# Kernel tuning notes

Hardware: AMD Instinct MI355X
Metric: run time of the kernel (lower is better)

Reference implementation:

```python
import jax, jax.numpy as jnp
import numpy as np

B, T, C = 8, 2048, 768
N_LAYER, LAYER_ID = 12, 0


def setup_inputs() -> dict:
    key = jax.random.key(0)
    ks = jax.random.split(key, 5)
    s = 1.0 / np.sqrt(C)
    x = jax.random.normal(ks[0], (B, T, C), jnp.float32)
    Wk = jax.random.normal(ks[1], (C, C), jnp.float32) * s
    Wv = jax.random.normal(ks[2], (C, C), jnp.float32) * s
    Wr = jax.random.normal(ks[3], (C, C), jnp.float32) * s
    Wo = jax.random.normal(ks[4], (C, C), jnp.float32) * s
    # 'fancy' init for decay / first (layer_id=0 -> ratio_0_to_1 = 0)
    h = np.arange(C, dtype=np.float64)
    decay = (-5.0 + 8.0 * (h / (C - 1)) ** 0.7).astype(np.float32)
    zigzag = (((np.arange(C) + 1) % 3) - 1).astype(np.float64) * 0.5
    first = (np.log(0.3) + zigzag).astype(np.float32)
    return dict(x=x, Wk=Wk, Wv=Wv, Wr=Wr, Wo=Wo,
                decay=jnp.asarray(decay), first=jnp.asarray(first))


def _bi_wkv(w, u, k, v):
    """Bidirectional WKV (Vision-RWKV style), numerically stabilized scans.

    y_t = (sum_{i<t} e^{-(t-1-i)w + k_i} v_i + sum_{i>t} e^{-(i-1-t)w + k_i} v_i
           + e^{u + k_t} v_t) / (same with v_i -> 1).
    k, v: [B,T,C]; w, u: [C].
    """
    kT = jnp.swapaxes(k, 0, 1)  # [T,B,C]
    vT = jnp.swapaxes(v, 0, 1)
    Bb, Cc = kT.shape[1], kT.shape[2]
    NEG = jnp.float32(-1e38)

    def step(carry, inp):
        a, b, p = carry  # a = sum e^{x_i-p} v_i, b = sum e^{x_i-p}, p = running max
        kt, vt = inp
        out = (a, b, p)  # state covers strictly-earlier positions
        p_new = jnp.maximum(p - w, kt)
        e1 = jnp.exp(p - w - p_new)
        e2 = jnp.exp(kt - p_new)
        return (e1 * a + e2 * vt, e1 * b + e2, p_new), out

    init = (jnp.zeros((Bb, Cc), jnp.float32),
            jnp.zeros((Bb, Cc), jnp.float32),
            jnp.full((Bb, Cc), NEG, jnp.float32))
    _, (aL, bL, pL) = jax.lax.scan(step, init, (kT, vT))
    _, (aR, bR, pR) = jax.lax.scan(step, init, (kT[::-1], vT[::-1]))
    aR, bR, pR = aR[::-1], bR[::-1], pR[::-1]

    ps = u + kT  # self term exponent
    q = jnp.maximum(jnp.maximum(pL, pR), ps)
    eL = jnp.exp(pL - q)
    eR = jnp.exp(pR - q)
    eS = jnp.exp(ps - q)
    y = (eL * aL + eR * aR + eS * vT) / (eL * bL + eR * bR + eS)
    return jnp.swapaxes(y, 0, 1)  # [B,T,C]


def reference(x, Wk, Wv, Wr, Wo, decay, first):
    Tlen = x.shape[1]
    # shift_pixel=0 -> xk = xv = xr = x
    k = jnp.einsum('btc,oc->bto', x, Wk)
    v = jnp.einsum('btc,oc->bto', x, Wv)
    sr = jax.nn.sigmoid(jnp.einsum('btc,oc->bto', x, Wr))
    y = _bi_wkv(decay / Tlen, first / Tlen, k, v)
    return jnp.einsum('btj,cj->btc', sr * y, Wo)
```

## Files before the change

### kernel.cpp

```cpp
#include <hip/hip_runtime.h>

#define BSZ 8
#define TLEN 2048
#define CDIM 768
#define LCH 16
#define NCH (TLEN / LCH)

typedef __attribute__((ext_vector_type(4))) float f32x4;
typedef __attribute__((ext_vector_type(8))) _Float16 f16x8;
typedef __attribute__((ext_vector_type(4))) _Float16 f16x4;
typedef __attribute__((ext_vector_type(4))) float float4v;

#define GLD16(g, l)                                                          \
    __builtin_amdgcn_global_load_lds(                                        \
        (const __attribute__((address_space(1))) unsigned int*)(g),          \
        (__attribute__((address_space(3))) unsigned int*)(l), 16, 0, 0)

__global__ __launch_bounds__(256) void split_f16(const float* __restrict__ src,
                                                 _Float16* __restrict__ dst, int n4) {
    int i = blockIdx.x * 256 + threadIdx.x;
    if (i >= n4) return;
    float4v f = ((const float4v*)src)[i];
    f16x4 h;
    #pragma unroll
    for (int j = 0; j < 4; ++j) h[j] = (_Float16)f[j];
    ((f16x4*)dst)[i] = h;
}

__global__ __launch_bounds__(512, 2) void gemm_8ph(
    const _Float16* __restrict__ A, const _Float16* __restrict__ W,
    _Float16* __restrict__ o0, _Float16* __restrict__ o1, _Float16* __restrict__ o2,
    float* __restrict__ of32, int mpx, int NTL) {
    constexpr int K = CDIM;
    constexpr int NT = K / 64;
    __shared__ __align__(16) char smem[131072];

    const int tid  = threadIdx.x;
    const int lane = tid & 63;
    const int wid  = tid >> 6;
    const int bid  = blockIdx.x;
    const int xcd  = bid & 7;
    const int lj   = bid >> 3;
    const int mt   = lj / NTL;
    const int nt   = lj - mt * NTL;
    const int m0   = (xcd * mpx + mt) * 256;
    const int n0   = nt * 256;

    const int r0 = tid >> 3;
    const int c0 = (tid & 7) ^ (r0 & 7);
    const int s1 = tid + 512;
    const int r1 = s1 >> 3;
    const int c1 = (s1 & 7) ^ (r1 & 7);
    const char* gA = (const char*)A;
    const char* gW = (const char*)W;

    auto STAGE_HALF = [&](int bufb, int q, int t) {
        const bool isA = (q < 2);
        const char* g = isA ? gA : gW;
        const int rowb = (isA ? m0 : n0) + (q & 1) * 128;
        char* l = &smem[bufb + q * 16384];
        GLD16(g + (size_t)((rowb + r0) * (K * 2) + c0 * 16 + t * 128), l + tid * 16);
        GLD16(g + (size_t)((rowb + r1) * (K * 2) + c1 * 16 + t * 128), l + s1 * 16);
    };

    const int wr = wid >> 2;
    const int wc = wid & 3;
    const int rl = lane & 15;
    const int kc0 = (((lane >> 4)    ) ^ (rl & 7)) << 4;
    const int kc1 = (((lane >> 4) + 4) ^ (rl & 7)) << 4;

    f32x4 acc[8][4];
    #pragma unroll
    for (int i = 0; i < 8; ++i)
        #pragma unroll
        for (int j = 0; j < 4; ++j)
            acc[i][j] = (f32x4){0.f, 0.f, 0.f, 0.f};

    #pragma unroll
    for (int q = 0; q < 4; ++q) STAGE_HALF(0, q, 0);
    asm volatile("s_waitcnt vmcnt(0)" ::: "memory");
    __builtin_amdgcn_s_barrier();

    for (int t = 0; t < NT; ++t) {
        const int db  = (t & 1) << 16;
        const int nb2 = db ^ 65536;
        const char* sb = &smem[db];
        f16x8 breg[4][2];

        #pragma unroll
        for (int q = 0; q < 4; ++q) {
            f16x8 areg[2][2];
            #pragma unroll
            for (int mi = 0; mi < 2; ++mi) {
                const int ro = (wr * 128 + (2 * q + mi) * 16 + rl) * 128;
                areg[mi][0] = *(const f16x8*)(sb + ro + kc0);
                areg[mi][1] = *(const f16x8*)(sb + ro + kc1);
            }
            if (q == 0) {
                #pragma unroll
                for (int nf = 0; nf < 4; ++nf) {
                    const int ro = 32768 + (wc * 64 + nf * 16 + rl) * 128;
                    breg[nf][0] = *(const f16x8*)(sb + ro + kc0);
                    breg[nf][1] = *(const f16x8*)(sb + ro + kc1);
                }
            }
            if (t + 1 < NT) STAGE_HALF(nb2, q, t + 1);

            __builtin_amdgcn_s_barrier();
            asm volatile("s_waitcnt lgkmcnt(0)" ::: "memory");
            __builtin_amdgcn_sched_barrier(0);
            __builtin_amdgcn_s_setprio(1);
            #pragma unroll
            for (int mi = 0; mi < 2; ++mi)
                #pragma unroll
                for (int nf = 0; nf < 4; ++nf) {
                    acc[2 * q + mi][nf] = __builtin_amdgcn_mfma_f32_16x16x32_f16(
                        areg[mi][0], breg[nf][0], acc[2 * q + mi][nf], 0, 0, 0);
                    acc[2 * q + mi][nf] = __builtin_amdgcn_mfma_f32_16x16x32_f16(
                        areg[mi][1], breg[nf][1], acc[2 * q + mi][nf], 0, 0, 0);
                }
            __builtin_amdgcn_s_setprio(0);
            if (q == 3) asm volatile("s_waitcnt vmcnt(0)" ::: "memory");
            __builtin_amdgcn_s_barrier();
        }
    }

    const int erow0 = m0 + wr * 128 + ((lane >> 4) << 2);
    if (of32) {
        const int col0 = n0 + wc * 64 + rl;
        #pragma unroll
        for (int mf = 0; mf < 8; ++mf)
            #pragma unroll
            for (int nf = 0; nf < 4; ++nf)
                #pragma unroll
                for (int r = 0; r < 4; ++r)
                    of32[(size_t)(erow0 + mf * 16 + r) * CDIM + (col0 + nf * 16)] =
                        acc[mf][nf][r];
    } else {
        const int mat  = nt / 3;
        const int col0 = (nt - mat * 3) * 256 + wc * 64 + rl;
        _Float16* o = (mat == 0) ? o0 : ((mat == 1) ? o1 : o2);
        if (mat == 2) {
            #pragma unroll
            for (int mf = 0; mf < 8; ++mf)
                #pragma unroll
                for (int nf = 0; nf < 4; ++nf)
                    #pragma unroll
                    for (int r = 0; r < 4; ++r)
                        o[(size_t)(erow0 + mf * 16 + r) * CDIM + (col0 + nf * 16)] =
                            (_Float16)(1.0f / (1.0f + __expf(-acc[mf][nf][r])));
        } else {
            #pragma unroll
            for (int mf = 0; mf < 8; ++mf)
                #pragma unroll
                for (int nf = 0; nf < 4; ++nf)
                    #pragma unroll
                    for (int r = 0; r < 4; ++r)
                        o[(size_t)(erow0 + mf * 16 + r) * CDIM + (col0 + nf * 16)] =
                            (_Float16)acc[mf][nf][r];
        }
    }
}

#define WKV_STEP(a, bb, p, kt, vt, w)                \
    {                                                \
        const float pn = fmaxf((p) - (w), (kt));     \
        const float e1 = __expf((p) - (w) - pn);     \
        const float e2 = __expf((kt) - pn);          \
        (a)  = e1 * (a)  + e2 * (vt);                \
        (bb) = e1 * (bb) + e2;                       \
        (p)  = pn;                                   \
    }

__global__ __launch_bounds__(256) void wkv_phase1(
    const _Float16* __restrict__ k, const _Float16* __restrict__ v,
    const float* __restrict__ decay,
    float* __restrict__ Sfa, float* __restrict__ Sfb, float* __restrict__ Sfp,
    float* __restrict__ Sba, float* __restrict__ Sbb, float* __restrict__ Sbp) {
    const int c = blockIdx.x * 256 + threadIdx.x;
    const int j = blockIdx.y;
    const int b = blockIdx.z;
    const float w = decay[c] * (1.0f / (float)TLEN);

    const size_t base = ((size_t)b * TLEN + (size_t)j * LCH) * CDIM + c;
    float kt[LCH], vt[LCH];
    #pragma unroll
    for (int i = 0; i < LCH; ++i) {
        kt[i] = (float)k[base + (size_t)i * CDIM];
        vt[i] = (float)v[base + (size_t)i * CDIM];
    }

    const size_t idx = ((size_t)b * NCH + j) * CDIM + c;

    float a = 0.0f, bb = 0.0f, p = -1e38f;
    #pragma unroll
    for (int i = 0; i < LCH; ++i) WKV_STEP(a, bb, p, kt[i], vt[i], w);
    Sfa[idx] = a; Sfb[idx] = bb; Sfp[idx] = p;

    a = 0.0f; bb = 0.0f; p = -1e38f;
    #pragma unroll
    for (int i = LCH - 1; i >= 0; --i) WKV_STEP(a, bb, p, kt[i], vt[i], w);
    Sba[idx] = a; Sbb[idx] = bb; Sbp[idx] = p;
}

#define WKV_COMBINE(a, bb, p, as, bs, ps, wL)        \
    {                                                \
        const float pn = fmaxf((p) - (wL), (ps));    \
        const float e1 = __expf((p) - (wL) - pn);    \
        const float e2 = __expf((ps) - pn);          \
        (a)  = e1 * (a)  + e2 * (as);                \
        (bb) = e1 * (bb) + e2 * (bs);                \
        (p)  = pn;                                   \
    }

__global__ __launch_bounds__(64) void wkv_phase2(
    const float* __restrict__ Sfa, const float* __restrict__ Sfb, const float* __restrict__ Sfp,
    const float* __restrict__ Sba, const float* __restrict__ Sbb, const float* __restrict__ Sbp,
    const float* __restrict__ decay,
    float* __restrict__ Lina, float* __restrict__ Linb, float* __restrict__ Linp,
    float* __restrict__ Rina, float* __restrict__ Rinb, float* __restrict__ Rinp) {
    const int c = blockIdx.x * 64 + threadIdx.x;
    const int b = blockIdx.y;
    const int dir = blockIdx.z;
    const float wL = decay[c] * ((float)LCH / (float)TLEN);

    const float* Sa = dir ? Sba : Sfa;
    const float* Sb = dir ? Sbb : Sfb;
    const float* Sp = dir ? Sbp : Sfp;
    float* Oa = dir ? Rina : Lina;
    float* Ob = dir ? Rinb : Linb;
    float* Op = dir ? Rinp : Linp;

    const size_t base = (size_t)b * NCH * CDIM + c;
    auto IDX = [&](int j) {
        return base + (size_t)(dir ? (NCH - 1 - j) : j) * CDIM;
    };

    float gaA[4], gbA[4], gpA[4], gaB[4], gbB[4], gpB[4];
    #pragma unroll
    for (int u = 0; u < 4; ++u) {
        const size_t id = IDX(u);
        gaA[u] = Sa[id]; gbA[u] = Sb[id]; gpA[u] = Sp[id];
    }
    float a = 0.0f, bb = 0.0f, p = -1e38f;

    for (int jg = 0; jg < NCH; jg += 8) {
        #pragma unroll
        for (int u = 0; u < 4; ++u) {
            const size_t id = IDX(jg + 4 + u);
            gaB[u] = Sa[id]; gbB[u] = Sb[id]; gpB[u] = Sp[id];
        }
        #pragma unroll
        for (int u = 0; u < 4; ++u) {
            const size_t id = IDX(jg + u);
            Oa[id] = a; Ob[id] = bb; Op[id] = p;
            WKV_COMBINE(a, bb, p, gaA[u], gbA[u], gpA[u], wL);
        }
        if (jg + 8 < NCH) {
            #pragma unroll
            for (int u = 0; u < 4; ++u) {
                const size_t id = IDX(jg + 8 + u);
                gaA[u] = Sa[id]; gbA[u] = Sb[id]; gpA[u] = Sp[id];
            }
        }
        #pragma unroll
        for (int u = 0; u < 4; ++u) {
            const size_t id = IDX(jg + 4 + u);
            Oa[id] = a; Ob[id] = bb; Op[id] = p;
            WKV_COMBINE(a, bb, p, gaB[u], gbB[u], gpB[u], wL);
        }
    }
}

__global__ __launch_bounds__(256) void wkv_phase3(
    const _Float16* __restrict__ k, const _Float16* __restrict__ v,
    const _Float16* __restrict__ sr,
    const float* __restrict__ Lina, const float* __restrict__ Linb, const float* __restrict__ Linp,
    const float* __restrict__ Rina, const float* __restrict__ Rinb, const float* __restrict__ Rinp,
    const float* __restrict__ decay, const float* __restrict__ first,
    _Float16* __restrict__ zh) {
    const int c = blockIdx.x * 256 + threadIdx.x;
    const int j = blockIdx.y;
    const int b = blockIdx.z;
    const float w = decay[c] * (1.0f / (float)TLEN);
    const float u = first[c] * (1.0f / (float)TLEN);

    const size_t base = ((size_t)b * TLEN + (size_t)j * LCH) * CDIM + c;
    float kt[LCH], vt[LCH];
    #pragma unroll
    for (int i = 0; i < LCH; ++i) {
        kt[i] = (float)k[base + (size_t)i * CDIM];
        vt[i] = (float)v[base + (size_t)i * CDIM];
    }

    const size_t idx = ((size_t)b * NCH + j) * CDIM + c;

    float ar[LCH], br[LCH], pr[LCH];
    {
        float a = Rina[idx], bb = Rinb[idx], p = Rinp[idx];
        #pragma unroll
        for (int i = LCH - 1; i >= 0; --i) {
            ar[i] = a; br[i] = bb; pr[i] = p;
            WKV_STEP(a, bb, p, kt[i], vt[i], w);
        }
    }
    {
        float a = Lina[idx], bb = Linb[idx], p = Linp[idx];
        #pragma unroll
        for (int i = 0; i < LCH; ++i) {
            const size_t off = base + (size_t)i * CDIM;
            const float srt = (float)sr[off];
            const float ps = u + kt[i];
            const float q  = fmaxf(fmaxf(p, pr[i]), ps);
            const float eL = __expf(p - q);
            const float eR = __expf(pr[i] - q);
            const float eS = __expf(ps - q);
            const float num = eL * a  + eR * ar[i] + eS * vt[i];
            const float den = eL * bb + eR * br[i] + eS;
            zh[off] = (_Float16)(srt * (num / den));
            WKV_STEP(a, bb, p, kt[i], vt[i], w);
        }
    }
}

extern "C" void kernel_launch(void* const* d_in, const int* in_sizes, int n_in,
                              void* d_out, int out_size, void* d_ws, size_t ws_size,
                              hipStream_t stream) {
    const float* x     = (const float*)d_in[0];
    const float* Wk    = (const float*)d_in[1];
    const float* Wv    = (const float*)d_in[2];
    const float* Wr    = (const float*)d_in[3];
    const float* Wo    = (const float*)d_in[4];
    const float* decay = (const float*)d_in[5];
    const float* first = (const float*)d_in[6];
    float* out = (float*)d_out;

    const size_t WN = (size_t)CDIM * CDIM;
    const size_t wbytes = 4 * WN * sizeof(_Float16);
    const size_t per_b  = (size_t)TLEN * CDIM * 8 + 12ull * NCH * CDIM * 4;
    if (ws_size < wbytes + per_b) return;
    int nb = (int)((ws_size - wbytes) / per_b);
    if (nb > BSZ) nb = BSZ;

    _Float16* wsp  = (_Float16*)d_ws;
    _Float16* Wcat = wsp;
    _Float16* Woh  = wsp + 3 * WN;

    const size_t NE = (size_t)nb * TLEN * CDIM;
    const size_t NP = (size_t)nb * NCH * CDIM;
    float* Sfa = (float*)(wsp + 4 * WN);
    float* Sfb = Sfa + NP;  float* Sfp = Sfb + NP;
    float* Sba = Sfp + NP;  float* Sbb = Sba + NP;  float* Sbp = Sbb + NP;
    float* Lina = Sbp + NP; float* Linb = Lina + NP; float* Linp = Linb + NP;
    float* Rina = Linp + NP; float* Rinb = Rina + NP; float* Rinp = Rinb + NP;
    _Float16* kh  = (_Float16*)(Rinp + NP);
    _Float16* vh  = kh + NE;
    _Float16* srh = vh + NE;
    _Float16* xh  = srh + NE;
    _Float16* zh  = xh;

    split_f16<<<dim3((int)(WN / 1024)), dim3(256), 0, stream>>>(Wk, Wcat + 0 * WN, (int)(WN / 4));
    split_f16<<<dim3((int)(WN / 1024)), dim3(256), 0, stream>>>(Wv, Wcat + 1 * WN, (int)(WN / 4));
    split_f16<<<dim3((int)(WN / 1024)), dim3(256), 0, stream>>>(Wr, Wcat + 2 * WN, (int)(WN / 4));
    split_f16<<<dim3((int)(WN / 1024)), dim3(256), 0, stream>>>(Wo, Woh, (int)(WN / 4));

    for (int b0 = 0; b0 < BSZ; b0 += nb) {
        const int curb = (BSZ - b0 < nb) ? (BSZ - b0) : nb;
        const int rows = curb * TLEN;
        const float* xc = x   + (size_t)b0 * TLEN * CDIM;
        float*       oc = out + (size_t)b0 * TLEN * CDIM;

        const int n4 = rows * CDIM / 4;
        split_f16<<<dim3(n4 / 256), dim3(256), 0, stream>>>(xc, xh, n4);

        const int mtiles = rows / 256;
        const int mpx    = mtiles / 8;

        gemm_8ph<<<dim3(mtiles * 9), dim3(512), 0, stream>>>(
            xh, Wcat, kh, vh, srh, nullptr, mpx, 9);

        wkv_phase1<<<dim3(CDIM / 256, NCH, curb), dim3(256), 0, stream>>>(
            kh, vh, decay, Sfa, Sfb, Sfp, Sba, Sbb, Sbp);
        wkv_phase2<<<dim3(CDIM / 64, curb, 2), dim3(64), 0, stream>>>(
            Sfa, Sfb, Sfp, Sba, Sbb, Sbp, decay,
            Lina, Linb, Linp, Rina, Rinb, Rinp);
        wkv_phase3<<<dim3(CDIM / 256, NCH, curb), dim3(256), 0, stream>>>(
            kh, vh, srh, Lina, Linb, Linp, Rina, Rinb, Rinp, decay, first, zh);

        gemm_8ph<<<dim3(mtiles * 3), dim3(512), 0, stream>>>(
            zh, Woh, nullptr, nullptr, nullptr, oc, mpx, 3);
    }
}
```

Before: 190.2 us.

## Restructure GEMM LDS layout into K-split sections with finer vmcnt waits

Changes the shared-memory tile layout from 128-byte swizzled rows to two 64-byte K-sections per operand, staged as separate A/W sections, and drops the XOR swizzle. Each phase now loads four A fragments and reuses B across the two M halves of a K-section. The end-of-tile full vmcnt(0) wait becomes a vmcnt(4) wait per phase, so later prefetches stay in flight. Unswizzled 64-byte rows may cause LDS bank conflicts on the fragment reads, and the partial-wait count must match the actual load ordering to stay correct.

```diff
diff --git a/kernel.cpp b/kernel.cpp
--- a/kernel.cpp
+++ b/kernel.cpp
@@ -46,28 +46,31 @@
     const int m0   = (xcd * mpx + mt) * 256;
     const int n0   = nt * 256;
 
-    const int r0 = tid >> 3;
-    const int c0 = (tid & 7) ^ (r0 & 7);
-    const int s1 = tid + 512;
-    const int r1 = s1 >> 3;
-    const int c1 = (s1 & 7) ^ (r1 & 7);
+    const int j0 = tid, j1 = tid + 512;
     const char* gA = (const char*)A;
     const char* gW = (const char*)W;
-
-    auto STAGE_HALF = [&](int bufb, int q, int t) {
-        const bool isA = (q < 2);
-        const char* g = isA ? gA : gW;
-        const int rowb = (isA ? m0 : n0) + (q & 1) * 128;
-        char* l = &smem[bufb + q * 16384];
-        GLD16(g + (size_t)((rowb + r0) * (K * 2) + c0 * 16 + t * 128), l + tid * 16);
-        GLD16(g + (size_t)((rowb + r1) * (K * 2) + c1 * 16 + t * 128), l + s1 * 16);
+    const size_t gA0 = (size_t)(m0 + (j0 >> 2)) * (K * 2) + (j0 & 3) * 16;
+    const size_t gA1 = (size_t)(m0 + (j1 >> 2)) * (K * 2) + (j1 & 3) * 16;
+    const size_t gW0 = (size_t)(n0 + (j0 >> 2)) * (K * 2) + (j0 & 3) * 16;
+    const size_t gW1 = (size_t)(n0 + (j1 >> 2)) * (K * 2) + (j1 & 3) * 16;
+
+    auto STAGE_SEC = [&](int bufb, int p, int t) {
+        const int ks = p >> 1;
+        const int secb = bufb + (p & 1) * 16384 + ks * 32768;
+        const size_t kb = (size_t)t * 128 + ks * 64;
+        if ((p & 1) == 0) {
+            GLD16(gA + gA0 + kb, &smem[secb] + j0 * 16);
+            GLD16(gA + gA1 + kb, &smem[secb] + j1 * 16);
+        } else {
+            GLD16(gW + gW0 + kb, &smem[secb] + j0 * 16);
+            GLD16(gW + gW1 + kb, &smem[secb] + j1 * 16);
+        }
     };
 
     const int wr = wid >> 2;
     const int wc = wid & 3;
     const int rl = lane & 15;
-    const int kc0 = (((lane >> 4)    ) ^ (rl & 7)) << 4;
-    const int kc1 = (((lane >> 4) + 4) ^ (rl & 7)) << 4;
+    const int kc = (lane >> 4) << 4;
 
     f32x4 acc[8][4];
     #pragma unroll
@@ -77,7 +80,7 @@
             acc[i][j] = (f32x4){0.f, 0.f, 0.f, 0.f};
 
     #pragma unroll
-    for (int q = 0; q < 4; ++q) STAGE_HALF(0, q, 0);
+    for (int p = 0; p < 4; ++p) STAGE_SEC(0, p, 0);
     asm volatile("s_waitcnt vmcnt(0)" ::: "memory");
     __builtin_amdgcn_s_barrier();
 
@@ -85,42 +88,38 @@
         const int db  = (t & 1) << 16;
         const int nb2 = db ^ 65536;
         const char* sb = &smem[db];
-        f16x8 breg[4][2];
-
-        #pragma unroll
-        for (int q = 0; q < 4; ++q) {
-            f16x8 areg[2][2];
-            #pragma unroll
-            for (int mi = 0; mi < 2; ++mi) {
-                const int ro = (wr * 128 + (2 * q + mi) * 16 + rl) * 128;
-                areg[mi][0] = *(const f16x8*)(sb + ro + kc0);
-                areg[mi][1] = *(const f16x8*)(sb + ro + kc1);
+        f16x8 breg[4];
+
+        #pragma unroll
+        for (int p = 0; p < 4; ++p) {
+            const int ks = p >> 1, mh = p & 1;
+            const char* asec = sb + ks * 32768;
+            const char* bsec = sb + 16384 + ks * 32768;
+
+            f16x8 areg[4];
+            #pragma unroll
+            for (int mi = 0; mi < 4; ++mi)
+                areg[mi] = *(const f16x8*)(asec + (wr * 128 + (mh * 4 + mi) * 16 + rl) * 64 + kc);
+            if (mh == 0) {
+                #pragma unroll
+                for (int nf = 0; nf < 4; ++nf)
+                    breg[nf] = *(const f16x8*)(bsec + (wc * 64 + nf * 16 + rl) * 64 + kc);
             }
-            if (q == 0) {
-                #pragma unroll
-                for (int nf = 0; nf < 4; ++nf) {
-                    const int ro = 32768 + (wc * 64 + nf * 16 + rl) * 128;
-                    breg[nf][0] = *(const f16x8*)(sb + ro + kc0);
-                    breg[nf][1] = *(const f16x8*)(sb + ro + kc1);
-                }
-            }
-            if (t + 1 < NT) STAGE_HALF(nb2, q, t + 1);
+            if (t + 1 < NT) STAGE_SEC(nb2, p, t + 1);
 
             __builtin_amdgcn_s_barrier();
             asm volatile("s_waitcnt lgkmcnt(0)" ::: "memory");
             __builtin_amdgcn_sched_barrier(0);
             __builtin_amdgcn_s_setprio(1);
             #pragma unroll
-            for (int mi = 0; mi < 2; ++mi)
-                #pragma unroll
-                for (int nf = 0; nf < 4; ++nf) {
-                    acc[2 * q + mi][nf] = __builtin_amdgcn_mfma_f32_16x16x32_f16(
-                        areg[mi][0], breg[nf][0], acc[2 * q + mi][nf], 0, 0, 0);
-                    acc[2 * q + mi][nf] = __builtin_amdgcn_mfma_f32_16x16x32_f16(
-                        areg[mi][1], breg[nf][1], acc[2 * q + mi][nf], 0, 0, 0);
-                }
+            for (int mi = 0; mi < 4; ++mi)
+                #pragma unroll
+                for (int nf = 0; nf < 4; ++nf)
+                    acc[mh * 4 + mi][nf] = __builtin_amdgcn_mfma_f32_16x16x32_f16(
+                        areg[mi], breg[nf], acc[mh * 4 + mi][nf], 0, 0, 0);
             __builtin_amdgcn_s_setprio(0);
-            if (q == 3) asm volatile("s_waitcnt vmcnt(0)" ::: "memory");
+            if (t + 1 < NT) asm volatile("s_waitcnt vmcnt(4)" ::: "memory");
+            else            asm volatile("s_waitcnt vmcnt(0)" ::: "memory");
             __builtin_amdgcn_s_barrier();
         }
     }
```

Result: no change. 191.3 us (+0.6%).
